# Performance work log

Hardware: AMD Instinct MI355X
Metric: run time of the kernel (lower is better)

Reference implementation:

```python
import jax, jax.numpy as jnp
import numpy as np

T, B, D = 256, 64, 1024  # time steps, batch (envs), hidden/input dim


def setup_inputs() -> dict:
    key = jax.random.key(0)
    ks = jax.random.split(key, 8)
    s = 1.0 / np.sqrt(D).astype(np.float32)  # lecun-normal-ish scale
    return {
        "ins": jax.random.normal(ks[0], (T, B, D), jnp.float32),
        "hiddens": jax.random.normal(ks[1], (T, B, D), jnp.float32),
        "dones": jax.random.randint(ks[2], (T, B), 0, 2).astype(bool),
        "init_carry": jax.random.normal(ks[3], (B, D), jnp.float32),
        # concatenated input->hidden weights [D, 3D] for (r, z, n) gates
        "W_i": jax.random.normal(ks[4], (D, 3 * D), jnp.float32) * s,
        # concatenated hidden->hidden weights [D, 3D] for (r, z, n) gates
        "W_h": jax.random.normal(ks[5], (D, 3 * D), jnp.float32) * s,
        # input-side biases (b_ir, b_iz, b_in)
        "b_i": jax.random.normal(ks[6], (3 * D,), jnp.float32) * 0.01,
        # hidden-side bias for the 'n' gate only (flax GRUCell: hn Dense has bias)
        "b_hn": jax.random.normal(ks[7], (D,), jnp.float32) * 0.01,
    }


def reference(ins, hiddens, dones, init_carry, W_i, W_h, b_i, b_hn):
    # Hoist input projections out of the scan (same math as per-step Dense)
    x_proj = jnp.einsum('tbd,de->tbe', ins, W_i) + b_i  # [T, B, 3D]
    xr, xz, xn = jnp.split(x_proj, 3, axis=-1)
    W_hr, W_hz, W_hn = jnp.split(W_h, 3, axis=1)

    def step(h, inp):
        xr_t, xz_t, xn_t, hid_t, done_t = inp
        # reset hidden state where episode terminated
        h = jnp.where(done_t[:, None], hid_t, h)
        r = jax.nn.sigmoid(xr_t + h @ W_hr)
        z = jax.nn.sigmoid(xz_t + h @ W_hz)
        n = jnp.tanh(xn_t + r * (h @ W_hn + b_hn))
        h_new = (1.0 - z) * n + z * h  # flax GRUCell update
        return h_new, h_new  # GRUCell returns (new_carry, new_carry)

    final_carry, ys = jax.lax.scan(step, init_carry, (xr, xz, xn, hiddens, dones))
    return final_carry, ys
```

## Files before the change

kernel.cpp:

```cpp
#include <hip/hip_runtime.h>
#include <hip/hip_bf16.h>
#include <stdint.h>


#define T_STEPS 256
#define NB 64
#define DIM 1024
#define NPH 32

typedef unsigned short u16;
typedef __attribute__((ext_vector_type(8))) short bf16x8;
typedef __attribute__((ext_vector_type(4))) float f32x4;

__device__ __forceinline__ float b2f(u16 u){ union{unsigned i; float f;} v; v.i=((unsigned)u)<<16; return v.f; }
__device__ __forceinline__ u16 f2b(float f){
  union { __hip_bfloat16 h; u16 u; } v; v.h = __float2bfloat16(f); return v.u;
}
__device__ __forceinline__ unsigned pk2(float lo, float hi){
  union { __hip_bfloat162 h; unsigned u; } v;
  v.h = __float22bfloat162_rn(make_float2(lo, hi));
  return v.u;
}
__device__ __forceinline__ float sigf(float x){ return 1.0f/(1.0f+__expf(-x)); }
__device__ __forceinline__ float tanh_f(float x){ float ax=fabsf(x); float e=__expf(-2.0f*ax); float t=(1.0f-e)/(1.0f+e); return copysignf(t,x); }

__device__ __forceinline__ void gl_lds16(const u16* g, u16* lbase, int lane){
#if __has_builtin(__builtin_amdgcn_global_load_lds)
  __builtin_amdgcn_global_load_lds(
      (const __attribute__((address_space(1))) unsigned int*)g,
      (__attribute__((address_space(3))) unsigned int*)lbase, 16, 0, 0);
#else
  *(uint4*)(lbase + lane*8) = *(const uint4*)g;
#endif
}

__device__ __forceinline__ int get_mode(const int* d){
  return (!d[0]) ? 0 : ((!d[1]) ? 3 : ((!d[2]) ? 2 : 1));
}
__device__ __forceinline__ int get_done(const void* dn, int mode, int i){
  if (mode == 0) return ((const int*)dn)[i] != 0;
  if (mode == 3) return ((const unsigned*)dn)[i] != 0;
  if (mode == 2) return ((const u16*)dn)[i] != 0;
  return ((const unsigned char*)dn)[i] != 0;
}

__global__ void k_setup0(const void* dones, const void* ins, int* cnt, int* cur, int* dflag){
  int tid = threadIdx.x;
  if (tid < NPH){ cnt[tid]=0; cur[tid]=0; }
  if (tid < 4) dflag[tid]=0;
  __syncthreads();
  const unsigned* di = (const unsigned*)dones;
  int vInt=0, vF32=0, vB16=0;
  for (int i = tid; i < 4096; i += 256){
    unsigned v = di[i];
    if (v > 1u) vInt = 1;
    if (v != 0u && v != 0x3F800000u) vF32 = 1;
    unsigned h0 = v & 0xFFFFu, h1 = v >> 16;
    if ((h0 != 0u && h0 != 0x3F80u) || (h1 != 0u && h1 != 0x3F80u)) vB16 = 1;
  }
  if (vInt) atomicOr(&dflag[0], 1);
  if (vF32) atomicOr(&dflag[1], 1);
  if (vB16) atomicOr(&dflag[2], 1);
  const u16* iu = (const u16*)ins;
  int f = 0;
  for (int i = tid; i < 4096; i += 256){
    u16 u = iu[2*i];
    if (((u >> 7) & 0xFF) >= 160) f = 1;
  }
  if (f) atomicOr(&dflag[3], 1);
}

__global__ void k_assign(const void* dones, const int* dflag, int* s_of, int* cnt){
  __shared__ unsigned char sd[T_STEPS];
  int b = blockIdx.x, t = threadIdx.x;
  int mode = get_mode(dflag);
  sd[t] = (unsigned char)get_done(dones, mode, t*NB + b);
  __syncthreads();
  int tt = t;
  while (tt > 0 && !sd[tt]) --tt;
  int s = t - tt;
  if (s >= NPH) s = NPH-1;
  s_of[t*NB + b] = s;
  atomicAdd(&cnt[s], 1);
}

__global__ void k_scan(const int* cnt, int* basep, int* cur){
  if (threadIdx.x == 0){
    int a = 0;
    for (int i=0;i<NPH;++i){ basep[i]=a; a += cnt[i]; }
    basep[NPH] = a;
  }
  if (threadIdx.x < NPH) cur[threadIdx.x] = 0;
}

__global__ void k_fill(const void* dones, const int* dflag, const int* s_of,
                       const int* basep, int* row_tb, int* row_src){
  int s = blockIdx.x;
  __shared__ int runbase;
  __shared__ int wsum[4];
  int tid = threadIdx.x, lane = tid & 63, wave = tid >> 6;
  int mode = get_mode(dflag);
  if (tid == 0) runbase = basep[s];
  __syncthreads();
  for (int i0 = 0; i0 < T_STEPS*NB; i0 += 256){
    int i = i0 + tid;
    int match = (s_of[i] == s);
    unsigned long long mask = __ballot(match);
    if (lane == 0) wsum[wave] = __popcll(mask);
    __syncthreads();
    int off = runbase;
    for (int w = 0; w < wave; ++w) off += wsum[w];
    int total = wsum[0] + wsum[1] + wsum[2] + wsum[3];
    if (match){
      int pos = off + __popcll(mask & ((1ull << lane) - 1ull));
      row_tb[pos] = i;
      int t = i >> 6, b = i & 63;
      int code;
      if (s > 0) code = (t-1)*NB + b;
      else if (get_done(dones, mode, i)) code = i | 0x40000000;
      else code = b | 0x20000000;
      row_src[pos] = code;
    }
    __syncthreads();
    if (tid == 0) runbase += total;
  }
}

__global__ void k_transpose(const void* __restrict__ W, u16* __restrict__ WT, const int* dflag){
  __shared__ u16 ts[64][65];
  int k0 = blockIdx.x*64, n0 = blockIdx.y*64, tid = threadIdx.x;
  int isf = dflag[3];
  for (int i = tid; i < 4096; i += 256){
    int r=i>>6, c=i&63; int idx=(k0+r)*3072 + n0 + c;
    ts[r][c] = isf ? f2b(((const float*)W)[idx]) : ((const u16*)W)[idx];
  }
  __syncthreads();
  for (int i = tid; i < 4096; i += 256){
    int r=i>>6, c=i&63;
    WT[(n0+r)*DIM + k0 + c] = ts[c][r];
  }
}

__global__ void k_bias(const void* bi, const void* bhn, const int* dflag,
                       u16* bi_b, u16* bhn_b){
  int isf = dflag[3];
  int i = blockIdx.x*256 + threadIdx.x;
  if (i < 3072) bi_b[i] = isf ? f2b(((const float*)bi)[i]) : ((const u16*)bi)[i];
  else { int j=i-3072; bhn_b[j] = isf ? f2b(((const float*)bhn)[j]) : ((const u16*)bhn)[j]; }
}

__device__ __forceinline__ void hsrc(int code, const void* outv, const void* hiddens,
                                     const void* initc, const void** hb, size_t* ho){
  if (code & 0x40000000){ *hb = hiddens; *ho = (size_t)(code & 0x0FFFFFFF)*DIM; }
  else if (code & 0x20000000){ *hb = initc; *ho = (size_t)(code & 0x0FFFFFFF)*DIM; }
  else { *hb = outv; *ho = (size_t)NB*DIM + (size_t)code*DIM; }
}

__global__ __launch_bounds__(256, 3) void k_xproj(
    const void* __restrict__ ins, const u16* __restrict__ WiT,
    const int* __restrict__ dflag, u16* __restrict__ xp)
{
  __shared__ u16 As[128*64];
  __shared__ u16 Bs[128*64];
  int isf = dflag[3];
  int tid=threadIdx.x, wave=tid>>6, lane=tid&63, quad=lane>>4, l16=lane&15;
  int wm=wave&1, wn=wave>>1;
  int srow = wave*8 + (lane>>3), c8=(lane&7)*8;
  int swzc = c8 ^ ((srow&7)<<3);
  int rsw = (l16&7)<<3;
  int tn = blockIdx.x % 24, tm = blockIdx.x / 24;
  f32x4 acc[4][4] = {};
  unsigned aoff[4], boff[4];
  #pragma unroll
  for (int p=0;p<4;++p){
    aoff[p] = (unsigned)(tm*128 + p*32 + srow)*DIM + c8;
    boff[p] = (unsigned)(tn*128 + p*32 + srow)*DIM + swzc;
  }
  f32x4 pr0[4], pr1[4];
  #pragma unroll
  for (int p=0;p<4;++p){
    if (isf){ const float* f=(const float*)ins + aoff[p]; pr0[p]=*(const f32x4*)f; pr1[p]=*(const f32x4*)(f+4); }
    else pr0[p]=*(const f32x4*)((const u16*)ins + aoff[p]);
  }
  #pragma unroll 1
  for (int ko=0; ko<1024; ko+=64){
    #pragma unroll
    for (int p=0;p<4;++p) gl_lds16(WiT + boff[p] + ko, &Bs[(p*32+wave*8)*64], lane);
    #pragma unroll
    for (int p=0;p<4;++p){
      uint4 w;
      if (isf){ w.x=pk2(pr0[p][0],pr0[p][1]); w.y=pk2(pr0[p][2],pr0[p][3]);
                w.z=pk2(pr1[p][0],pr1[p][1]); w.w=pk2(pr1[p][2],pr1[p][3]); }
      else { union{f32x4 f; uint4 u;} cv; cv.f=pr0[p]; w=cv.u; }
      *(uint4*)&As[(p*32+srow)*64 + swzc] = w;
    }
    __syncthreads();
    if (ko < 960){
      #pragma unroll
      for (int p=0;p<4;++p){
        if (isf){ const float* f=(const float*)ins + aoff[p] + ko + 64; pr0[p]=*(const f32x4*)f; pr1[p]=*(const f32x4*)(f+4); }
        else pr0[p]=*(const f32x4*)((const u16*)ins + aoff[p] + ko + 64);
      }
    }
    #pragma unroll
    for (int kk=0;kk<64;kk+=32){
      int rc = (kk + quad*8) ^ rsw;
      bf16x8 af[4], bfv[4];
      #pragma unroll
      for (int mi=0;mi<4;++mi) af[mi]  = *(const bf16x8*)&As[(wm*64+mi*16+l16)*64 + rc];
      #pragma unroll
      for (int ni=0;ni<4;++ni) bfv[ni] = *(const bf16x8*)&Bs[(wn*64+ni*16+l16)*64 + rc];
      #pragma unroll
      for (int mi=0;mi<4;++mi)
        #pragma unroll
        for (int ni=0;ni<4;++ni)
          acc[mi][ni] = __builtin_amdgcn_mfma_f32_16x16x32_bf16(af[mi],bfv[ni],acc[mi][ni],0,0,0);
    }
    __syncthreads();
  }
  #pragma unroll
  for (int mi=0;mi<4;++mi){
    int row = tm*128 + wm*64 + mi*16 + quad*4;
    #pragma unroll
    for (int ni=0;ni<4;++ni){
      int colB = tn*128 + wn*64 + ni*16 + l16;
      u16* op = xp + (size_t)row*3072 + colB;
      #pragma unroll
      for (int j=0;j<4;++j)
        op[(size_t)j*3072] = f2b(acc[mi][ni][j]);
    }
  }
}

#define FAT_PANEL(BASEARR, OFFARR, WT, NGRP)                                   \
    {                                                                          \
      f32x4 pr0[4], pr1[4];                                                    \
      _Pragma("unroll")                                                        \
      for (int p=0;p<4;++p){                                                   \
        if (isf){ const float* f=(const float*)BASEARR[p]+OFFARR[p];           \
          pr0[p]=*(const f32x4*)f; pr1[p]=*(const f32x4*)(f+4); }              \
        else pr0[p]=*(const f32x4*)((const u16*)BASEARR[p]+OFFARR[p]);         \
      }                                                                        \
      _Pragma("unroll 1")                                                      \
      for (int ko=0; ko<1024; ko+=64){                                         \
        _Pragma("unroll")                                                      \
        for (int p=0;p<3;++p)                                                  \
          gl_lds16(WT + boff[p] + ko, &Bs[(p*32+wave*8)*64], lane);            \
        _Pragma("unroll")                                                      \
        for (int p=0;p<4;++p){                                                 \
          uint4 w;                                                             \
          if (isf){ w.x=pk2(pr0[p][0],pr0[p][1]); w.y=pk2(pr0[p][2],pr0[p][3]);\
                    w.z=pk2(pr1[p][0],pr1[p][1]); w.w=pk2(pr1[p][2],pr1[p][3]);}\
          else { union{f32x4 f; uint4 u;} cv; cv.f=pr0[p]; w=cv.u; }           \
          *(uint4*)&As[(p*32+srow)*64 + swzc] = w;                             \
        }                                                                      \
        __syncthreads();                                                       \
        if (ko < 960){                                                         \
          _Pragma("unroll")                                                    \
          for (int p=0;p<4;++p){                                               \
            if (isf){ const float* f=(const float*)BASEARR[p]+OFFARR[p]+ko+64; \
              pr0[p]=*(const f32x4*)f; pr1[p]=*(const f32x4*)(f+4); }          \
            else pr0[p]=*(const f32x4*)((const u16*)BASEARR[p]+OFFARR[p]+ko+64);\
          }                                                                    \
        }                                                                      \
        _Pragma("unroll")                                                      \
        for (int kk=0;kk<64;kk+=32){                                           \
          int rc = (kk + quad*8) ^ rsw;                                        \
          bf16x8 af[4];                                                        \
          _Pragma("unroll")                                                    \
          for (int mi=0;mi<4;++mi)                                             \
            af[mi] = *(const bf16x8*)&As[(wm*64+mi*16+l16)*64 + rc];           \
          _Pragma("unroll")                                                    \
          for (int g=0;g<3;++g){                                               \
            bf16x8 bfr = *(const bf16x8*)&Bs[(g*32+wn*16+l16)*64 + rc];        \
            int grp = (g==2) ? (NGRP) : g;                                     \
            _Pragma("unroll")                                                  \
            for (int mi=0;mi<4;++mi)                                           \
              acc[mi][grp] = __builtin_amdgcn_mfma_f32_16x16x32_bf16(af[mi],bfr,acc[mi][grp],0,0,0); \
          }                                                                    \
        }                                                                      \
        __syncthreads();                                                       \
      }                                                                        \
    }

template<bool HOIST>
__global__ __launch_bounds__(256, 3) void phase_fat(
    int s, const int* __restrict__ pcnt, const int* __restrict__ pbase,
    const int* __restrict__ row_tb, const int* __restrict__ row_src,
    const void* __restrict__ ins, const void* __restrict__ hiddens,
    const void* __restrict__ initc, const u16* __restrict__ WiT,
    const u16* __restrict__ WhT, const u16* __restrict__ bi_b,
    const u16* __restrict__ bhn_b, const int* __restrict__ dflag,
    const u16* __restrict__ xp, void* __restrict__ outv)
{
  int count = pcnt[s];
  if (count <= 0) return;
  int isf = dflag[3];
  int base = pbase[s];
  int mtiles = (count + 127) >> 7;
  int ntot = mtiles << 5;
  __shared__ u16 As[128*64];
  __shared__ u16 Bs[96*64];
  int tid=threadIdx.x, wave=tid>>6, lane=tid&63, quad=lane>>4, l16=lane&15;
  int wm=wave&1, wn=wave>>1;
  int srow = wave*8 + (lane>>3), c8=(lane&7)*8;
  int swzc = c8 ^ ((srow&7)<<3);
  int rsw = (l16&7)<<3;
  constexpr int NG = HOIST ? 3 : 4;

  for (int tile = blockIdx.x; tile < ntot; tile += gridDim.x){
    int tm = tile >> 5, dblk = tile & 31, d0 = dblk*32;
    unsigned xoff[4], hoff[4];
    const void* hbv[4];
    const void* xbv[4];
    #pragma unroll
    for (int p=0;p<4;++p){
      int lr = tm*128 + p*32 + srow;
      int idx = base + ((lr < count) ? lr : 0);
      int tb = row_tb[idx], code = row_src[idx];
      xoff[p] = (unsigned)tb*DIM + c8;
      xbv[p] = ins;
      size_t ho; const void* hb;
      hsrc(code, outv, hiddens, initc, &hb, &ho);
      hbv[p] = hb; hoff[p] = (unsigned)ho + c8;
    }
    int boff[3];
    #pragma unroll
    for (int p=0;p<3;++p) boff[p] = (p*DIM + d0 + srow)*DIM + swzc;
    f32x4 acc[4][NG] = {};

    if constexpr (!HOIST){
      FAT_PANEL(xbv, xoff, WiT, 2)
    }
    FAT_PANEL(hbv, hoff, WhT, (NG-1))

    int col = d0 + wn*16 + l16;
    float br = b2f(bi_b[col]), bz = b2f(bi_b[1024+col]);
    float bn = b2f(bi_b[2048+col]), bh = b2f(bhn_b[col]);
    #pragma unroll
    for (int mi=0;mi<4;++mi){
      int lrow0 = tm*128 + wm*64 + mi*16 + quad*4;
      #pragma unroll
      for (int j=0;j<4;++j){
        int lrow = lrow0 + j;
        if (lrow >= count) continue;
        int idx = base + lrow;
        int tb = row_tb[idx], code = row_src[idx];
        size_t ho; const void* hb;
        hsrc(code, outv, hiddens, initc, &hb, &ho);
        float hpv = isf ? ((const float*)hb)[ho + col] : b2f(((const u16*)hb)[ho + col]);
        float xr = 0.f, xz = 0.f, xn = 0.f;
        if constexpr (HOIST){
          const u16* xrow = xp + (size_t)tb*3072 + col;
          xr = b2f(xrow[0]); xz = b2f(xrow[1024]); xn = b2f(xrow[2048]);
        }
        float r = sigf(br + xr + acc[mi][0][j]);
        float z = sigf(bz + xz + acc[mi][1][j]);
        float nx = HOIST ? xn : acc[mi][2][j];
        float n = tanh_f(bn + nx + r*(acc[mi][NG-1][j] + bh));
        float hnew = (1.0f - z)*n + z*hpv;
        size_t yo = (size_t)NB*DIM + (size_t)tb*DIM + col;
        if (isf) ((float*)outv)[yo] = hnew;
        else     ((u16*)outv)[yo] = f2b(hnew);
      }
    }
  }
}

#define THIN_PANEL(BASEARR, OFFARR, WT, NGRP)                                  \
    {                                                                          \
      f32x4 pr0[2], pr1[2];                                                    \
      _Pragma("unroll")                                                        \
      for (int p=0;p<2;++p){                                                   \
        if (isf){ const float* f=(const float*)BASEARR[p]+OFFARR[p];           \
          pr0[p]=*(const f32x4*)f; pr1[p]=*(const f32x4*)(f+4); }              \
        else pr0[p]=*(const f32x4*)((const u16*)BASEARR[p]+OFFARR[p]);         \
      }                                                                        \
      _Pragma("unroll 1")                                                      \
      for (int ko=0; ko<1024; ko+=64){                                         \
        gl_lds16(WT + boffA + ko, &Bs[(wave*8)*64], lane);                     \
        if (wave < 2) gl_lds16(WT + boffB + ko, &Bs[(32+wave*8)*64], lane);    \
        _Pragma("unroll")                                                      \
        for (int p=0;p<2;++p){                                                 \
          uint4 w;                                                             \
          if (isf){ w.x=pk2(pr0[p][0],pr0[p][1]); w.y=pk2(pr0[p][2],pr0[p][3]);\
                    w.z=pk2(pr1[p][0],pr1[p][1]); w.w=pk2(pr1[p][2],pr1[p][3]);}\
          else { union{f32x4 f; uint4 u;} cv; cv.f=pr0[p]; w=cv.u; }           \
          *(uint4*)&As[(p*32+srow)*64 + swzc] = w;                             \
        }                                                                      \
        __syncthreads();                                                       \
        if (ko < 960){                                                         \
          _Pragma("unroll")                                                    \
          for (int p=0;p<2;++p){                                               \
            if (isf){ const float* f=(const float*)BASEARR[p]+OFFARR[p]+ko+64; \
              pr0[p]=*(const f32x4*)f; pr1[p]=*(const f32x4*)(f+4); }          \
            else pr0[p]=*(const f32x4*)((const u16*)BASEARR[p]+OFFARR[p]+ko+64);\
          }                                                                    \
        }                                                                      \
        _Pragma("unroll")                                                      \
        for (int kk=0;kk<64;kk+=32){                                           \
          int rc = (kk + quad*8) ^ rsw;                                        \
          bf16x8 af = *(const bf16x8*)&As[(wave*16+l16)*64 + rc];              \
          _Pragma("unroll")                                                    \
          for (int g=0;g<3;++g){                                               \
            bf16x8 bfr = *(const bf16x8*)&Bs[(g*16+l16)*64 + rc];              \
            int grp = (g==2) ? (NGRP) : g;                                     \
            acc[grp] = __builtin_amdgcn_mfma_f32_16x16x32_bf16(af,bfr,acc[grp],0,0,0); \
          }                                                                    \
        }                                                                      \
        __syncthreads();                                                       \
      }                                                                        \
    }

template<bool HOIST>
__global__ __launch_bounds__(256, 4) void phase_thin(
    int s, const int* __restrict__ pcnt, const int* __restrict__ pbase,
    const int* __restrict__ row_tb, const int* __restrict__ row_src,
    const void* __restrict__ ins, const void* __restrict__ hiddens,
    const void* __restrict__ initc, const u16* __restrict__ WiT,
    const u16* __restrict__ WhT, const u16* __restrict__ bi_b,
    const u16* __restrict__ bhn_b, const int* __restrict__ dflag,
    const u16* __restrict__ xp, void* __restrict__ outv)
{
  int count = pcnt[s];
  if (count <= 0) return;
  int isf = dflag[3];
  int base = pbase[s];
  int mtiles = (count + 63) >> 6;
  int ntot = mtiles << 6;
  __shared__ u16 As[64*64];
  __shared__ u16 Bs[48*64];
  int tid=threadIdx.x, wave=tid>>6, lane=tid&63, quad=lane>>4, l16=lane&15;
  int srow = wave*8 + (lane>>3), c8=(lane&7)*8;
  int swzc = c8 ^ ((srow&7)<<3);
  int rsw = (l16&7)<<3;
  constexpr int NG = HOIST ? 3 : 4;

  for (int tile = blockIdx.x; tile < ntot; tile += gridDim.x){
    int tm = tile >> 6, dblk = tile & 63, d0 = dblk*16;
    unsigned xoff[2], hoff[2];
    const void* hbv[2];
    const void* xbv[2];
    #pragma unroll
    for (int p=0;p<2;++p){
      int lr = tm*64 + p*32 + srow;
      int idx = base + ((lr < count) ? lr : 0);
      int tb = row_tb[idx], code = row_src[idx];
      xoff[p] = (unsigned)tb*DIM + c8;
      xbv[p] = ins;
      size_t ho; const void* hb;
      hsrc(code, outv, hiddens, initc, &hb, &ho);
      hbv[p] = hb; hoff[p] = (unsigned)ho + c8;
    }
    int boffA = ((srow>>4)*DIM + d0 + (srow&15))*DIM + swzc;
    int boffB = (2*DIM + d0 + srow)*DIM + swzc;
    f32x4 acc[NG] = {};

    if constexpr (!HOIST){
      THIN_PANEL(xbv, xoff, WiT, 2)
    }
    THIN_PANEL(hbv, hoff, WhT, (HOIST ? 2 : 3))

    int col = d0 + l16;
    float br = b2f(bi_b[col]), bz = b2f(bi_b[1024+col]);
    float bn = b2f(bi_b[2048+col]), bh = b2f(bhn_b[col]);
    int lrow0 = tm*64 + wave*16 + quad*4;
    #pragma unroll
    for (int j=0;j<4;++j){
      int lrow = lrow0 + j;
      if (lrow >= count) continue;
      int idx = base + lrow;
      int tb = row_tb[idx], code = row_src[idx];
      size_t ho; const void* hb;
      hsrc(code, outv, hiddens, initc, &hb, &ho);
      float hpv = isf ? ((const float*)hb)[ho + col] : b2f(((const u16*)hb)[ho + col]);
      float xr = 0.f, xz = 0.f, xn = 0.f;
      if constexpr (HOIST){
        const u16* xrow = xp + (size_t)tb*3072 + col;
        xr = b2f(xrow[0]); xz = b2f(xrow[1024]); xn = b2f(xrow[2048]);
      }
      float r = sigf(br + xr + acc[0][j]);
      float z = sigf(bz + xz + acc[1][j]);
      float nx = HOIST ? xn : acc[2][j];
      float n = tanh_f(bn + nx + r*(acc[NG-1][j] + bh));
      float hnew = (1.0f - z)*n + z*hpv;
      size_t yo = (size_t)NB*DIM + (size_t)tb*DIM + col;
      if (isf) ((float*)outv)[yo] = hnew;
      else     ((u16*)outv)[yo] = f2b(hnew);
    }
  }
}

__global__ void k_final(const int* dflag, void* out){
  int isf = dflag[3];
  size_t i = (size_t)(blockIdx.x*256 + threadIdx.x)*4;
  size_t src = (size_t)NB*DIM + (size_t)(T_STEPS-1)*NB*DIM;
  if (isf){
    float* o = (float*)out;
    *(f32x4*)(o + i) = *(const f32x4*)(o + src + i);
  } else {
    u16* o = (u16*)out;
    *(uint2*)(o + i) = *(const uint2*)(o + src + i);
  }
}

extern "C" void kernel_launch(void* const* d_in, const int* in_sizes, int n_in,
                              void* d_out, int out_size, void* d_ws, size_t ws_size,
                              hipStream_t stream){
  const void* ins = d_in[0];
  const void* hid = d_in[1];
  const void* dn  = d_in[2];
  const void* ini = d_in[3];
  const void* Wi  = d_in[4];
  const void* Wh  = d_in[5];
  const void* bi  = d_in[6];
  const void* bhn = d_in[7];

  char* ws = (char*)d_ws;
  int* dflag  = (int*)(ws + 0);
  int* cnt    = (int*)(ws + 256);
  int* basep  = (int*)(ws + 512);
  int* cur    = (int*)(ws + 1024);
  int* s_of   = (int*)(ws + 4096);
  int* row_tb = (int*)(ws + 69632);
  int* row_src= (int*)(ws + 135168);
  u16* bi_b   = (u16*)(ws + 200704);
  u16* bhn_b  = (u16*)(ws + 208896);
  u16* WiT    = (u16*)(ws + 262144);
  u16* WhT    = (u16*)(ws + 6553600);
  u16* xp     = (u16*)(ws + 12845056);

  const int hoist = (ws_size >= 113508352ull) ? 1 : 0;

  k_setup0<<<1,256,0,stream>>>(dn, ins, cnt, cur, dflag);
  k_assign<<<NB,T_STEPS,0,stream>>>(dn, dflag, s_of, cnt);
  k_scan<<<1,64,0,stream>>>(cnt, basep, cur);
  k_fill<<<NPH,256,0,stream>>>(dn, dflag, s_of, basep, row_tb, row_src);
  k_transpose<<<dim3(16,48),256,0,stream>>>(Wi, WiT, dflag);
  k_transpose<<<dim3(16,48),256,0,stream>>>(Wh, WhT, dflag);
  k_bias<<<16,256,0,stream>>>(bi, bhn, dflag, bi_b, bhn_b);

  if (hoist){
    k_xproj<<<3072,256,0,stream>>>(ins, WiT, dflag, xp);
    for (int s=0;s<6;++s)
      phase_fat<true><<<1024,256,0,stream>>>(s, cnt, basep, row_tb, row_src, ins, hid, ini,
                                             WiT, WhT, bi_b, bhn_b, dflag, xp, d_out);
    for (int s=6;s<NPH;++s)
      phase_thin<true><<<128,256,0,stream>>>(s, cnt, basep, row_tb, row_src, ins, hid, ini,
                                             WiT, WhT, bi_b, bhn_b, dflag, xp, d_out);
  } else {
    for (int s=0;s<6;++s)
      phase_fat<false><<<1024,256,0,stream>>>(s, cnt, basep, row_tb, row_src, ins, hid, ini,
                                              WiT, WhT, bi_b, bhn_b, dflag, xp, d_out);
    for (int s=6;s<NPH;++s)
      phase_thin<false><<<128,256,0,stream>>>(s, cnt, basep, row_tb, row_src, ins, hid, ini,
                                              WiT, WhT, bi_b, bhn_b, dflag, xp, d_out);
  }
  k_final<<<64,256,0,stream>>>(dflag, d_out);
}
```

Baseline: 1.128 ms.

## Double-buffer LDS tiles in GEMM kernels, widen fat tiles, add XCD-aware block swizzle

Converts the xproj, fat-phase and thin-phase GEMM loops to double-buffered shared memory, so the next K-slice is loaded while the current one feeds MFMA, with one barrier per iteration instead of two. The fat phase doubles its N tile from 32 to 64 columns per gate, which reuses each A fragment across more MFMAs. Block indices are remapped so neighbouring tiles land on the same XCD for L2 locality. The cost is twice the LDS footprint and a lower launch-bounds occupancy target (3 to 2 blocks per CU).

```diff
diff --git a/kernel.cpp b/kernel.cpp
--- a/kernel.cpp
+++ b/kernel.cpp
@@ -23,6 +23,13 @@
 }
 __device__ __forceinline__ float sigf(float x){ return 1.0f/(1.0f+__expf(-x)); }
 __device__ __forceinline__ float tanh_f(float x){ float ax=fabsf(x); float e=__expf(-2.0f*ax); float t=(1.0f-e)/(1.0f+e); return copysignf(t,x); }
+
+__device__ __forceinline__ int xcdswz(int raw, int n){
+  int xcd = raw & 7, idx = raw >> 3;
+  int q = n >> 3, r = n & 7;
+  int base = (xcd < r) ? xcd*(q+1) : r*(q+1) + (xcd-r)*q;
+  return base + idx;
+}
 
 __device__ __forceinline__ void gl_lds16(const u16* g, u16* lbase, int lane){
 #if __has_builtin(__builtin_amdgcn_global_load_lds)
@@ -32,6 +39,20 @@
 #else
   *(uint4*)(lbase + lane*8) = *(const uint4*)g;
 #endif
+}
+
+__device__ __forceinline__ void stage16(const void* base, size_t eoff, int isf, u16* dst){
+  if (isf){
+    const float* f = (const float*)base + eoff;
+    f32x4 a0 = *(const f32x4*)f;
+    f32x4 a1 = *(const f32x4*)(f+4);
+    uint4 w;
+    w.x = pk2(a0[0],a0[1]); w.y = pk2(a0[2],a0[3]);
+    w.z = pk2(a1[0],a1[1]); w.w = pk2(a1[2],a1[3]);
+    *(uint4*)dst = w;
+  } else {
+    *(uint4*)dst = *(const uint4*)((const u16*)base + eoff);
+  }
 }
 
 __device__ __forceinline__ int get_mode(const int* d){
@@ -156,19 +177,20 @@
   else { *hb = outv; *ho = (size_t)NB*DIM + (size_t)code*DIM; }
 }
 
-__global__ __launch_bounds__(256, 3) void k_xproj(
+__global__ __launch_bounds__(256, 2) void k_xproj(
     const void* __restrict__ ins, const u16* __restrict__ WiT,
     const int* __restrict__ dflag, u16* __restrict__ xp)
 {
-  __shared__ u16 As[128*64];
-  __shared__ u16 Bs[128*64];
+  __shared__ u16 As[2][128*64];
+  __shared__ u16 Bs[2][128*64];
   int isf = dflag[3];
   int tid=threadIdx.x, wave=tid>>6, lane=tid&63, quad=lane>>4, l16=lane&15;
   int wm=wave&1, wn=wave>>1;
   int srow = wave*8 + (lane>>3), c8=(lane&7)*8;
   int swzc = c8 ^ ((srow&7)<<3);
   int rsw = (l16&7)<<3;
-  int tn = blockIdx.x % 24, tm = blockIdx.x / 24;
+  int l = xcdswz(blockIdx.x, 3072);
+  int tn = l % 24, tm = l / 24;
   f32x4 acc[4][4] = {};
   unsigned aoff[4], boff[4];
   #pragma unroll
@@ -176,47 +198,60 @@
     aoff[p] = (unsigned)(tm*128 + p*32 + srow)*DIM + c8;
     boff[p] = (unsigned)(tn*128 + p*32 + srow)*DIM + swzc;
   }
-  f32x4 pr0[4], pr1[4];
   #pragma unroll
-  for (int p=0;p<4;++p){
-    if (isf){ const float* f=(const float*)ins + aoff[p]; pr0[p]=*(const f32x4*)f; pr1[p]=*(const f32x4*)(f+4); }
-    else pr0[p]=*(const f32x4*)((const u16*)ins + aoff[p]);
-  }
+  for (int p=0;p<4;++p) gl_lds16(WiT + boff[p], &Bs[0][(p*32+wave*8)*64], lane);
+  #pragma unroll
+  for (int p=0;p<4;++p) stage16(ins, aoff[p], isf, &As[0][(p*32+srow)*64 + swzc]);
+  __syncthreads();
+  int cur = 0;
   #pragma unroll 1
-  for (int ko=0; ko<1024; ko+=64){
-    #pragma unroll
-    for (int p=0;p<4;++p) gl_lds16(WiT + boff[p] + ko, &Bs[(p*32+wave*8)*64], lane);
+  for (int ko=64; ko<1024; ko+=64){
+    #pragma unroll
+    for (int p=0;p<4;++p) gl_lds16(WiT + boff[p] + ko, &Bs[cur^1][(p*32+wave*8)*64], lane);
+    f32x4 pr0[4], pr1[4];
+    #pragma unroll
+    for (int p=0;p<4;++p){
+      if (isf){ const float* f=(const float*)ins + aoff[p] + ko; pr0[p]=*(const f32x4*)f; pr1[p]=*(const f32x4*)(f+4); }
+      else pr0[p]=*(const f32x4*)((const u16*)ins + aoff[p] + ko);
+    }
+    #pragma unroll
+    for (int kk=0;kk<64;kk+=32){
+      int rc = (kk + quad*8) ^ rsw;
+      bf16x8 af[4], bfv[4];
+      #pragma unroll
+      for (int mi=0;mi<4;++mi) af[mi]  = *(const bf16x8*)&As[cur][(wm*64+mi*16+l16)*64 + rc];
+      #pragma unroll
+      for (int ni=0;ni<4;++ni) bfv[ni] = *(const bf16x8*)&Bs[cur][(wn*64+ni*16+l16)*64 + rc];
+      #pragma unroll
+      for (int mi=0;mi<4;++mi)
+        #pragma unroll
+        for (int ni=0;ni<4;++ni)
+          acc[mi][ni] = __builtin_amdgcn_mfma_f32_16x16x32_bf16(af[mi],bfv[ni],acc[mi][ni],0,0,0);
+    }
     #pragma unroll
     for (int p=0;p<4;++p){
       uint4 w;
       if (isf){ w.x=pk2(pr0[p][0],pr0[p][1]); w.y=pk2(pr0[p][2],pr0[p][3]);
                 w.z=pk2(pr1[p][0],pr1[p][1]); w.w=pk2(pr1[p][2],pr1[p][3]); }
       else { union{f32x4 f; uint4 u;} cv; cv.f=pr0[p]; w=cv.u; }
-      *(uint4*)&As[(p*32+srow)*64 + swzc] = w;
+      *(uint4*)&As[cur^1][(p*32+srow)*64 + swzc] = w;
     }
     __syncthreads();
-    if (ko < 960){
+    cur ^= 1;
+  }
+  #pragma unroll
+  for (int kk=0;kk<64;kk+=32){
+    int rc = (kk + quad*8) ^ rsw;
+    bf16x8 af[4], bfv[4];
+    #pragma unroll
+    for (int mi=0;mi<4;++mi) af[mi]  = *(const bf16x8*)&As[cur][(wm*64+mi*16+l16)*64 + rc];
+    #pragma unroll
+    for (int ni=0;ni<4;++ni) bfv[ni] = *(const bf16x8*)&Bs[cur][(wn*64+ni*16+l16)*64 + rc];
+    #pragma unroll
+    for (int mi=0;mi<4;++mi)
       #pragma unroll
-      for (int p=0;p<4;++p){
-        if (isf){ const float* f=(const float*)ins + aoff[p] + ko + 64; pr0[p]=*(const f32x4*)f; pr1[p]=*(const f32x4*)(f+4); }
-        else pr0[p]=*(const f32x4*)((const u16*)ins + aoff[p] + ko + 64);
-      }
-    }
-    #pragma unroll
-    for (int kk=0;kk<64;kk+=32){
-      int rc = (kk + quad*8) ^ rsw;
-      bf16x8 af[4], bfv[4];
-      #pragma unroll
-      for (int mi=0;mi<4;++mi) af[mi]  = *(const bf16x8*)&As[(wm*64+mi*16+l16)*64 + rc];
-      #pragma unroll
-      for (int ni=0;ni<4;++ni) bfv[ni] = *(const bf16x8*)&Bs[(wn*64+ni*16+l16)*64 + rc];
-      #pragma unroll
-      for (int mi=0;mi<4;++mi)
-        #pragma unroll
-        for (int ni=0;ni<4;++ni)
-          acc[mi][ni] = __builtin_amdgcn_mfma_f32_16x16x32_bf16(af[mi],bfv[ni],acc[mi][ni],0,0,0);
-    }
-    __syncthreads();
+      for (int ni=0;ni<4;++ni)
+        acc[mi][ni] = __builtin_amdgcn_mfma_f32_16x16x32_bf16(af[mi],bfv[ni],acc[mi][ni],0,0,0);
   }
   #pragma unroll
   for (int mi=0;mi<4;++mi){
@@ -232,59 +267,67 @@
   }
 }
 
-#define FAT_PANEL(BASEARR, OFFARR, WT, NGRP)                                   \
+#define FAT_MFMA(BUF, NGRP)                                                    \
+        _Pragma("unroll")                                                      \
+        for (int kk=0;kk<64;kk+=32){                                           \
+          int rc = (kk + quad*8) ^ rsw;                                        \
+          bf16x8 af[4];                                                        \
+          _Pragma("unroll")                                                    \
+          for (int mi=0;mi<4;++mi)                                             \
+            af[mi] = *(const bf16x8*)&As[BUF][(wm*64+mi*16+l16)*64 + rc];      \
+          _Pragma("unroll")                                                    \
+          for (int g=0;g<3;++g){                                               \
+            int grp = (g==2) ? (NGRP) : g;                                     \
+            _Pragma("unroll")                                                  \
+            for (int ni=0;ni<2;++ni){                                          \
+              bf16x8 bfr = *(const bf16x8*)&Bs[BUF][(g*64+wn*32+ni*16+l16)*64 + rc]; \
+              _Pragma("unroll")                                                \
+              for (int mi=0;mi<4;++mi)                                         \
+                acc[grp][mi][ni] = __builtin_amdgcn_mfma_f32_16x16x32_bf16(af[mi],bfr,acc[grp][mi][ni],0,0,0); \
+            }                                                                  \
+          }                                                                    \
+        }
+
+#define FAT_PANEL(BASEARR, OFFARR, WTP, NGRP)                                  \
     {                                                                          \
-      f32x4 pr0[4], pr1[4];                                                    \
+      __syncthreads();                                                         \
       _Pragma("unroll")                                                        \
-      for (int p=0;p<4;++p){                                                   \
-        if (isf){ const float* f=(const float*)BASEARR[p]+OFFARR[p];           \
-          pr0[p]=*(const f32x4*)f; pr1[p]=*(const f32x4*)(f+4); }              \
-        else pr0[p]=*(const f32x4*)((const u16*)BASEARR[p]+OFFARR[p]);         \
-      }                                                                        \
+      for (int p=0;p<6;++p)                                                    \
+        gl_lds16(WTP + boffB[p], &Bs[0][(p*32+wave*8)*64], lane);              \
+      _Pragma("unroll")                                                        \
+      for (int p=0;p<4;++p)                                                    \
+        stage16(BASEARR[p], OFFARR[p], isf, &As[0][(p*32+srow)*64 + swzc]);    \
+      __syncthreads();                                                         \
+      int cur = 0;                                                             \
       _Pragma("unroll 1")                                                      \
-      for (int ko=0; ko<1024; ko+=64){                                         \
+      for (int ko=64; ko<1024; ko+=64){                                        \
         _Pragma("unroll")                                                      \
-        for (int p=0;p<3;++p)                                                  \
-          gl_lds16(WT + boff[p] + ko, &Bs[(p*32+wave*8)*64], lane);            \
+        for (int p=0;p<6;++p)                                                  \
+          gl_lds16(WTP + boffB[p] + ko, &Bs[cur^1][(p*32+wave*8)*64], lane);   \
+        f32x4 pr0[4], pr1[4];                                                  \
+        _Pragma("unroll")                                                      \
+        for (int p=0;p<4;++p){                                                 \
+          if (isf){ const float* f=(const float*)BASEARR[p]+OFFARR[p]+ko;      \
+            pr0[p]=*(const f32x4*)f; pr1[p]=*(const f32x4*)(f+4); }            \
+          else pr0[p]=*(const f32x4*)((const u16*)BASEARR[p]+OFFARR[p]+ko);    \
+        }                                                                      \
+        FAT_MFMA(cur, NGRP)                                                    \
         _Pragma("unroll")                                                      \
         for (int p=0;p<4;++p){                                                 \
           uint4 w;                                                             \
           if (isf){ w.x=pk2(pr0[p][0],pr0[p][1]); w.y=pk2(pr0[p][2],pr0[p][3]);\
                     w.z=pk2(pr1[p][0],pr1[p][1]); w.w=pk2(pr1[p][2],pr1[p][3]);}\
           else { union{f32x4 f; uint4 u;} cv; cv.f=pr0[p]; w=cv.u; }           \
-          *(uint4*)&As[(p*32+srow)*64 + swzc] = w;                             \
+          *(uint4*)&As[cur^1][(p*32+srow)*64 + swzc] = w;                      \
         }                                                                      \
         __syncthreads();                                                       \
-        if (ko < 960){                                                         \
-          _Pragma("unroll")                                                    \
-          for (int p=0;p<4;++p){                                               \
-            if (isf){ const float* f=(const float*)BASEARR[p]+OFFARR[p]+ko+64; \
-              pr0[p]=*(const f32x4*)f; pr1[p]=*(const f32x4*)(f+4); }          \
-            else pr0[p]=*(const f32x4*)((const u16*)BASEARR[p]+OFFARR[p]+ko+64);\
-          }                                                                    \
-        }                                                                      \
-        _Pragma("unroll")                                                      \
-        for (int kk=0;kk<64;kk+=32){                                           \
-          int rc = (kk + quad*8) ^ rsw;                                        \
-          bf16x8 af[4];                                                        \
-          _Pragma("unroll")                                                    \
-          for (int mi=0;mi<4;++mi)                                             \
-            af[mi] = *(const bf16x8*)&As[(wm*64+mi*16+l16)*64 + rc];           \
-          _Pragma("unroll")                                                    \
-          for (int g=0;g<3;++g){                                               \
-            bf16x8 bfr = *(const bf16x8*)&Bs[(g*32+wn*16+l16)*64 + rc];        \
-            int grp = (g==2) ? (NGRP) : g;                                     \
-            _Pragma("unroll")                                                  \
-            for (int mi=0;mi<4;++mi)                                           \
-              acc[mi][grp] = __builtin_amdgcn_mfma_f32_16x16x32_bf16(af[mi],bfr,acc[mi][grp],0,0,0); \
-          }                                                                    \
-        }                                                                      \
-        __syncthreads();                                                       \
+        cur ^= 1;                                                              \
       }                                                                        \
+      FAT_MFMA(cur, NGRP)                                                      \
     }
 
 template<bool HOIST>
-__global__ __launch_bounds__(256, 3) void phase_fat(
+__global__ __launch_bounds__(256, 2) void phase_fat(
     int s, const int* __restrict__ pcnt, const int* __restrict__ pbase,
     const int* __restrict__ row_tb, const int* __restrict__ row_src,
     const void* __restrict__ ins, const void* __restrict__ hiddens,
@@ -298,9 +341,9 @@
   int isf = dflag[3];
   int base = pbase[s];
   int mtiles = (count + 127) >> 7;
-  int ntot = mtiles << 5;
-  __shared__ u16 As[128*64];
-  __shared__ u16 Bs[96*64];
+  int ntot = mtiles << 4;
+  __shared__ u16 As[2][128*64];
+  __shared__ u16 Bs[2][192*64];
   int tid=threadIdx.x, wave=tid>>6, lane=tid&63, quad=lane>>4, l16=lane&15;
   int wm=wave&1, wn=wave>>1;
   int srow = wave*8 + (lane>>3), c8=(lane&7)*8;
@@ -308,8 +351,9 @@
   int rsw = (l16&7)<<3;
   constexpr int NG = HOIST ? 3 : 4;
 
-  for (int tile = blockIdx.x; tile < ntot; tile += gridDim.x){
-    int tm = tile >> 5, dblk = tile & 31, d0 = dblk*32;
+  for (int raw = blockIdx.x; raw < ntot; raw += gridDim.x){
+    int tile = xcdswz(raw, ntot);
+    int tm = tile >> 4, dblk = tile & 15, d0 = dblk*64;
     unsigned xoff[4], hoff[4];
     const void* hbv[4];
     const void* xbv[4];
@@ -324,19 +368,25 @@
       hsrc(code, outv, hiddens, initc, &hb, &ho);
       hbv[p] = hb; hoff[p] = (unsigned)ho + c8;
     }
-    int boff[3];
-    #pragma unroll
-    for (int p=0;p<3;++p) boff[p] = (p*DIM + d0 + srow)*DIM + swzc;
-    f32x4 acc[4][NG] = {};
+    int boffB[6];
+    #pragma unroll
+    for (int p=0;p<6;++p)
+      boffB[p] = ((p>>1)*DIM + d0 + (p&1)*32 + srow)*DIM + swzc;
+    f32x4 acc[NG][4][2] = {};
 
     if constexpr (!HOIST){
       FAT_PANEL(xbv, xoff, WiT, 2)
     }
     FAT_PANEL(hbv, hoff, WhT, (NG-1))
 
-    int col = d0 + wn*16 + l16;
-    float br = b2f(bi_b[col]), bz = b2f(bi_b[1024+col]);
-    float bn = b2f(bi_b[2048+col]), bh = b2f(bhn_b[col]);
+    int col0 = d0 + wn*32;
+    float brv[2], bzv[2], bnv[2], bhv[2];
+    #pragma unroll
+    for (int ni=0;ni<2;++ni){
+      int c = col0 + ni*16 + l16;
+      brv[ni]=b2f(bi_b[c]); bzv[ni]=b2f(bi_b[1024+c]);
+      bnv[ni]=b2f(bi_b[2048+c]); bhv[ni]=b2f(bhn_b[c]);
+    }
     #pragma unroll
     for (int mi=0;mi<4;++mi){
       int lrow0 = tm*128 + wm*64 + mi*16 + quad*4;
@@ -348,68 +398,75 @@
         int tb = row_tb[idx], code = row_src[idx];
         size_t ho; const void* hb;
         hsrc(code, outv, hiddens, initc, &hb, &ho);
-        float hpv = isf ? ((const float*)hb)[ho + col] : b2f(((const u16*)hb)[ho + col]);
-        float xr = 0.f, xz = 0.f, xn = 0.f;
-        if constexpr (HOIST){
-          const u16* xrow = xp + (size_t)tb*3072 + col;
-          xr = b2f(xrow[0]); xz = b2f(xrow[1024]); xn = b2f(xrow[2048]);
+        #pragma unroll
+        for (int ni=0;ni<2;++ni){
+          int c = col0 + ni*16 + l16;
+          float hpv = isf ? ((const float*)hb)[ho + c] : b2f(((const u16*)hb)[ho + c]);
+          float xr = 0.f, xz = 0.f, xn = 0.f;
+          if constexpr (HOIST){
+            const u16* xrow = xp + (size_t)tb*3072 + c;
+            xr = b2f(xrow[0]); xz = b2f(xrow[1024]); xn = b2f(xrow[2048]);
+          }
+          float r = sigf(brv[ni] + xr + acc[0][mi][ni][j]);
+          float z = sigf(bzv[ni] + xz + acc[1][mi][ni][j]);
+          float nx = HOIST ? xn : acc[2][mi][ni][j];
+          float n = tanh_f(bnv[ni] + nx + r*(acc[NG-1][mi][ni][j] + bhv[ni]));
+          float hnew = (1.0f - z)*n + z*hpv;
+          size_t yo = (size_t)NB*DIM + (size_t)tb*DIM + c;
+          if (isf) ((float*)outv)[yo] = hnew;
+          else     ((u16*)outv)[yo] = f2b(hnew);
         }
-        float r = sigf(br + xr + acc[mi][0][j]);
-        float z = sigf(bz + xz + acc[mi][1][j]);
-        float nx = HOIST ? xn : acc[mi][2][j];
-        float n = tanh_f(bn + nx + r*(acc[mi][NG-1][j] + bh));
-        float hnew = (1.0f - z)*n + z*hpv;
-        size_t yo = (size_t)NB*DIM + (size_t)tb*DIM + col;
-        if (isf) ((float*)outv)[yo] = hnew;
-        else     ((u16*)outv)[yo] = f2b(hnew);
       }
     }
   }
 }
 
-#define THIN_PANEL(BASEARR, OFFARR, WT, NGRP)                                  \
+#define THIN_MFMA(BUF, NGRP)                                                   \
+      _Pragma("unroll")                                                        \
+      for (int kk=0;kk<64;kk+=32){                                             \
+        int rc = (kk + quad*8) ^ rsw;                                          \
+        bf16x8 af = *(const bf16x8*)&As[BUF][(wave*16+l16)*64 + rc];           \
+        _Pragma("unroll")                                                      \
+        for (int g=0;g<3;++g){                                                 \
+          bf16x8 bfr = *(const bf16x8*)&Bs[BUF][(g*16+l16)*64 + rc];           \
+          int grp = (g==2) ? (NGRP) : g;                                       \
+          acc[grp] = __builtin_amdgcn_mfma_f32_16x16x32_bf16(af,bfr,acc[grp],0,0,0); \
+        }                                                                      \
+      }
+
+#define THIN_PANEL(BASEARR, OFFARR, WTP, NGRP)                                 \
     {                                                                          \
-      f32x4 pr0[2], pr1[2];                                                    \
-      _Pragma("unroll")                                                        \
-      for (int p=0;p<2;++p){                                                   \
-        if (isf){ const float* f=(const float*)BASEARR[p]+OFFARR[p];           \
-          pr0[p]=*(const f32x4*)f; pr1[p]=*(const f32x4*)(f+4); }              \
-        else pr0[p]=*(const f32x4*)((const u16*)BASEARR[p]+OFFARR[p]);         \
-      }                                                                        \
+      __syncthreads();                                                         \
+      gl_lds16(WTP + boffA, &Bs[0][(wave*8)*64], lane);                        \
+      if (wave < 2) gl_lds16(WTP + boffC, &Bs[0][(32+wave*8)*64], lane);       \
+      stage16(BASEARR[0], OFFARR[0], isf, &As[0][srow*64 + swzc]);             \
+      stage16(BASEARR[1], OFFARR[1], isf, &As[0][(32+srow)*64 + swzc]);        \
+      __syncthreads();                                                         \
+      int cur = 0;                                                             \
       _Pragma("unroll 1")                                                      \
-      for (int ko=0; ko<1024; ko+=64){                                         \
-        gl_lds16(WT + boffA + ko, &Bs[(wave*8)*64], lane);                     \
-        if (wave < 2) gl_lds16(WT + boffB + ko, &Bs[(32+wave*8)*64], lane);    \
+      for (int ko=64; ko<1024; ko+=64){                                        \
+        gl_lds16(WTP + boffA + ko, &Bs[cur^1][(wave*8)*64], lane);             \
+        if (wave < 2) gl_lds16(WTP + boffC + ko, &Bs[cur^1][(32+wave*8)*64], lane); \
+        f32x4 pr0[2], pr1[2];                                                  \
+        _Pragma("unroll")                                                      \
+        for (int p=0;p<2;++p){                                                 \
+          if (isf){ const float* f=(const float*)BASEARR[p]+OFFARR[p]+ko;      \
+            pr0[p]=*(const f32x4*)f; pr1[p]=*(const f32x4*)(f+4); }            \
+          else pr0[p]=*(const f32x4*)((const u16*)BASEARR[p]+OFFARR[p]+ko);    \
+        }                                                                      \
+        THIN_MFMA(cur, NGRP)                                                   \
         _Pragma("unroll")                                                      \
         for (int p=0;p<2;++p){                                                 \
           uint4 w;                                                             \
           if (isf){ w.x=pk2(pr0[p][0],pr0[p][1]); w.y=pk2(pr0[p][2],pr0[p][3]);\
                     w.z=pk2(pr1[p][0],pr1[p][1]); w.w=pk2(pr1[p][2],pr1[p][3]);}\
           else { union{f32x4 f; uint4 u;} cv; cv.f=pr0[p]; w=cv.u; }           \
-          *(uint4*)&As[(p*32+srow)*64 + swzc] = w;                             \
+          *(uint4*)&As[cur^1][(p*32+srow)*64 + swzc] = w;                      \
         }                                                                      \
         __syncthreads();                                                       \
-        if (ko < 960){                                                         \
-          _Pragma("unroll")                                                    \
-          for (int p=0;p<2;++p){                                               \
-            if (isf){ const float* f=(const float*)BASEARR[p]+OFFARR[p]+ko+64; \
-              pr0[p]=*(const f32x4*)f; pr1[p]=*(const f32x4*)(f+4); }          \
-            else pr0[p]=*(const f32x4*)((const u16*)BASEARR[p]+OFFARR[p]+ko+64);\
-          }                                                                    \
-        }                                                                      \
-        _Pragma("unroll")                                                      \
-        for (int kk=0;kk<64;kk+=32){                                           \
-          int rc = (kk + quad*8) ^ rsw;                                        \
-          bf16x8 af = *(const bf16x8*)&As[(wave*16+l16)*64 + rc];              \
-          _Pragma("unroll")                                                    \
-          for (int g=0;g<3;++g){                                               \
-            bf16x8 bfr = *(const bf16x8*)&Bs[(g*16+l16)*64 + rc];              \
-            int grp = (g==2) ? (NGRP) : g;                                     \
-            acc[grp] = __builtin_amdgcn_mfma_f32_16x16x32_bf16(af,bfr,acc[grp],0,0,0); \
-          }                                                                    \
-        }                                                                      \
-        __syncthreads();                                                       \
+        cur ^= 1;                                                              \
       }                                                                        \
+      THIN_MFMA(cur, NGRP)                                                     \
     }
 
 template<bool HOIST>
@@ -428,8 +485,8 @@
   int base = pbase[s];
   int mtiles = (count + 63) >> 6;
   int ntot = mtiles << 6;
-  __shared__ u16 As[64*64];
-  __shared__ u16 Bs[48*64];
+  __shared__ u16 As[2][64*64];
+  __shared__ u16 Bs[2][48*64];
   int tid=threadIdx.x, wave=tid>>6, lane=tid&63, quad=lane>>4, l16=lane&15;
   int srow = wave*8 + (lane>>3), c8=(lane&7)*8;
   int swzc = c8 ^ ((srow&7)<<3);
@@ -453,7 +510,7 @@
       hbv[p] = hb; hoff[p] = (unsigned)ho + c8;
     }
     int boffA = ((srow>>4)*DIM + d0 + (srow&15))*DIM + swzc;
-    int boffB = (2*DIM + d0 + srow)*DIM + swzc;
+    int boffC = (2*DIM + d0 + srow)*DIM + swzc;
     f32x4 acc[NG] = {};
 
     if constexpr (!HOIST){
```

Result: slower. 1.165 ms (+3.3%).
